# Optimization experiments

Hardware: AMD Instinct MI355X
Metric: run time of the kernel (lower is better)

Reference implementation:

```python
import jax, jax.numpy as jnp
import numpy as np

D, H, HD, F, L, V, R = 4096, 32, 128, 11008, 2, 32002, 64
ALPHA = 16.0
B, S = 2, 1024
EPS = 1e-5


def setup_inputs() -> dict:
    key = jax.random.key(0)
    ks = jax.random.split(key, 24)
    n = lambda k, shape: (jax.random.normal(k, shape, jnp.float32) * 0.02)
    return {
        "input_ids": jax.random.randint(ks[0], (B, S), 0, V),
        "attention_mask": jnp.ones((B, S), jnp.int32),
        "embed": n(ks[1], (V, D)),
        "Wq": n(ks[2], (L, D, D)), "Wk": n(ks[3], (L, D, D)),
        "Wv": n(ks[4], (L, D, D)), "Wo": n(ks[5], (L, D, D)),
        "Aq": n(ks[6], (L, R, D)), "Bq": jnp.zeros((L, D, R), jnp.float32),
        "Ak": n(ks[7], (L, R, D)), "Bk": n(ks[8], (L, D, R)),
        "Av": n(ks[9], (L, R, D)), "Bv": n(ks[10], (L, D, R)),
        "Ao": n(ks[11], (L, R, D)), "Bo": n(ks[12], (L, D, R)),
        "Wgate": n(ks[13], (L, F, D)), "Wup": n(ks[14], (L, F, D)),
        "Wdown": n(ks[15], (L, D, F)),
        "attn_norm_w": jnp.ones((L, D), jnp.float32),
        "mlp_norm_w": jnp.ones((L, D), jnp.float32),
        "final_norm_w": jnp.ones((D,), jnp.float32),
        "cls_W": n(ks[16], (3, D)), "cls_b": jnp.zeros((3,), jnp.float32),
    }


def _rmsnorm(x, w):
    var = jnp.mean(jnp.square(x), axis=-1, keepdims=True)
    return (x * jax.lax.rsqrt(var + EPS)) * w


def _rope(seq_len):
    inv = 1.0 / (10000.0 ** (jnp.arange(0, HD, 2, dtype=jnp.float32) / HD))
    freqs = jnp.outer(jnp.arange(seq_len, dtype=jnp.float32), inv)  # [S, HD/2]
    emb = jnp.concatenate([freqs, freqs], -1)  # [S, HD]
    return jnp.cos(emb), jnp.sin(emb)


def _rot_half(x):
    h = x.shape[-1] // 2
    return jnp.concatenate([-x[..., h:], x[..., :h]], -1)


def _lora(h, W, A, Bm):
    # h @ W.T + (alpha/r) * (h @ A.T) @ B.T   (dropout inactive in eval)
    return h @ W.T + (h @ A.T) @ Bm.T * (ALPHA / R)


def reference(input_ids, attention_mask, embed, Wq, Wk, Wv, Wo,
              Aq, Bq, Ak, Bk, Av, Bv, Ao, Bo,
              Wgate, Wup, Wdown, attn_norm_w, mlp_norm_w, final_norm_w,
              cls_W, cls_b):
    b, s = input_ids.shape
    x = embed[input_ids]  # [B,S,D]
    cos, sin = _rope(s)  # [S,HD]
    causal = jnp.tril(jnp.ones((s, s), bool))
    mask = causal[None, None] & (attention_mask[:, None, None, :] > 0)
    bias = jnp.where(mask, 0.0, -1e9).astype(jnp.float32)  # [B,1,S,S]

    def heads(t):  # [B,S,D] -> [B,H,S,HD]
        return t.reshape(b, s, H, HD).transpose(0, 2, 1, 3)

    for l in range(L):
        h = _rmsnorm(x, attn_norm_w[l])
        q = heads(_lora(h, Wq[l], Aq[l], Bq[l]))
        k = heads(_lora(h, Wk[l], Ak[l], Bk[l]))
        v = heads(_lora(h, Wv[l], Av[l], Bv[l]))
        q = q * cos + _rot_half(q) * sin
        k = k * cos + _rot_half(k) * sin
        scores = jnp.einsum('bhqd,bhkd->bhqk', q, k) / np.sqrt(HD) + bias
        attn = jax.nn.softmax(scores, axis=-1)
        o = jnp.einsum('bhqk,bhkd->bhqd', attn, v)
        o = o.transpose(0, 2, 1, 3).reshape(b, s, D)
        x = x + _lora(o, Wo[l], Ao[l], Bo[l])
        h = _rmsnorm(x, mlp_norm_w[l])
        x = x + (jax.nn.silu(h @ Wgate[l].T) * (h @ Wup[l].T)) @ Wdown[l].T

    x = _rmsnorm(x, final_norm_w)
    cls = x[:, 0, :]  # [CLS] at position 0 (right padding)
    return cls @ cls_W.T + cls_b
```

## Files before the change

### kernel.cpp

```cpp
#include <hip/hip_runtime.h>
#include <cstdint>
#include <cstddef>

#define D_   4096
#define H_   32
#define HD_  128
#define F_   11008
#define L_   2
#define R_   64
#define BB   2
#define SS   1024
#define TOK  (BB*SS)
#define N3   12288
#define EPS_ 1e-5f

typedef __attribute__((ext_vector_type(8))) short          s16x8;
typedef __attribute__((ext_vector_type(4))) float          fx4;
typedef __attribute__((ext_vector_type(4))) unsigned short u16x4t;
typedef __attribute__((ext_vector_type(8))) unsigned short u16x8t;

__device__ __forceinline__ unsigned short f2bf(float f) {
  union { float f; unsigned u; } x; x.f = f;
  unsigned r = (x.u + 0x7FFFu + ((x.u >> 16) & 1u)) >> 16;
  return (unsigned short)r;
}
__device__ __forceinline__ float b2f(unsigned short h) {
  union { unsigned u; float f; } x; x.u = ((unsigned)h) << 16;
  return x.f;
}

__device__ __forceinline__ void xcd_remap(int nwg, int mt_cnt, int& mt, int& nt) {
  const int orig = blockIdx.x;
  const int q = nwg >> 3, r = nwg & 7;
  const int xcd = orig & 7, i = orig >> 3;
  const int wgid = (xcd < r ? xcd * (q + 1) : r * (q + 1) + (xcd - r) * q) + i;
  mt = wgid % mt_cnt;
  nt = wgid / mt_cnt;
}

__global__ void k_embed(const int* __restrict__ ids, const float* __restrict__ emb,
                        float* __restrict__ x) {
  const int tok = blockIdx.x, tid = threadIdx.x;
  const int id = ids[tok];
  const float* s = emb + (size_t)id * D_;
  float* d = x + (size_t)tok * D_;
#pragma unroll
  for (int i = 0; i < 4; ++i)
    *(fx4*)(d + i * 1024 + tid * 4) = *(const fx4*)(s + i * 1024 + tid * 4);
}

__global__ __launch_bounds__(256) void k_cvt(const float* __restrict__ src,
                                             unsigned short* __restrict__ dst, int n) {
  const int stride = gridDim.x * 256 * 8;
  for (int i = (blockIdx.x * 256 + threadIdx.x) * 8; i < n; i += stride) {
    fx4 a = *(const fx4*)(src + i);
    fx4 b = *(const fx4*)(src + i + 4);
    u16x8t p;
    p[0] = f2bf(a[0]); p[1] = f2bf(a[1]); p[2] = f2bf(a[2]); p[3] = f2bf(a[3]);
    p[4] = f2bf(b[0]); p[5] = f2bf(b[1]); p[6] = f2bf(b[2]); p[7] = f2bf(b[3]);
    *(u16x8t*)(dst + i) = p;
  }
}

__global__ __launch_bounds__(256) void k_rmsnorm(const float* __restrict__ x,
                                                 const float* __restrict__ w,
                                                 unsigned short* __restrict__ out) {
  const int row = blockIdx.x, tid = threadIdx.x;
  const float* xr = x + (size_t)row * D_;
  fx4 v[4];
  float ss = 0.f;
#pragma unroll
  for (int i = 0; i < 4; ++i) {
    v[i] = *(const fx4*)(xr + i * 1024 + tid * 4);
    ss += v[i][0]*v[i][0] + v[i][1]*v[i][1] + v[i][2]*v[i][2] + v[i][3]*v[i][3];
  }
#pragma unroll
  for (int off = 32; off > 0; off >>= 1) ss += __shfl_down(ss, off);
  __shared__ float red[4];
  if ((tid & 63) == 0) red[tid >> 6] = ss;
  __syncthreads();
  const float sc = rsqrtf((red[0] + red[1] + red[2] + red[3]) * (1.f / D_) + EPS_);
  unsigned short* orow = out + (size_t)row * D_;
#pragma unroll
  for (int i = 0; i < 4; ++i) {
    fx4 wv = *(const fx4*)(w + i * 1024 + tid * 4);
    u16x4t pk;
    pk.x = f2bf(v[i][0] * sc * wv[0]);
    pk.y = f2bf(v[i][1] * sc * wv[1]);
    pk.z = f2bf(v[i][2] * sc * wv[2]);
    pk.w = f2bf(v[i][3] * sc * wv[3]);
    *(u16x4t*)(orow + i * 1024 + tid * 4) = pk;
  }
}

__global__ __launch_bounds__(256) void k_merge(const float* __restrict__ W,
                                               const float* __restrict__ Al,
                                               const float* __restrict__ Bl,
                                               unsigned short* __restrict__ Wm, int Kd) {
  __shared__ float sBm[64 * 64];
  __shared__ float sAl[64 * 68];
  const int tid = threadIdx.x;
  const int n0 = blockIdx.y * 64, k0 = blockIdx.x * 64;
#pragma unroll
  for (int it = 0; it < 4; ++it) {
    int e = it * 1024 + tid * 4;
    int row = e >> 6, col = e & 63;
    *(fx4*)&sBm[row * 64 + col] = *(const fx4*)(Bl + (size_t)(n0 + row) * 64 + col);
    *(fx4*)&sAl[row * 68 + col] = *(const fx4*)(Al + (size_t)row * Kd + k0 + col);
  }
  __syncthreads();
  const int lane = tid & 63, wave = tid >> 6;
  for (int nn = 0; nn < 16; ++nn) {
    int n = wave * 16 + nn;
    float a = 0.f;
#pragma unroll
    for (int r = 0; r < 64; ++r) a += sBm[n * 64 + r] * sAl[r * 68 + lane];
    size_t gi = (size_t)(n0 + n) * Kd + k0 + lane;
    Wm[gi] = f2bf(W[gi] + 0.25f * a);
  }
}

template <int EPI>
__global__ __launch_bounds__(256, 4) void k_gemm(const unsigned short* __restrict__ A,
                                                 const unsigned short* __restrict__ Wb,
                                                 float* __restrict__ outF,
                                                 unsigned short* __restrict__ outB,
                                                 const float* __restrict__ auxF,
                                                 int M, int N, int K, int nwg) {
  __shared__ unsigned short sA[128 * 64];
  __shared__ unsigned short sB[128 * 64];
  const int tid = threadIdx.x;
  const int wave = tid >> 6, lane = tid & 63;
  int mt, nt;
  xcd_remap(nwg, M >> 7, mt, nt);
  const int m0 = mt * 128, n0 = nt * 128;
  const int wr = wave >> 1, wc = wave & 1;
  const int l15 = lane & 15, l4 = lane >> 4;

  fx4 acc[4][4];
#pragma unroll
  for (int i = 0; i < 4; ++i)
#pragma unroll
    for (int j = 0; j < 4; ++j) acc[i][j] = (fx4){0.f, 0.f, 0.f, 0.f};

  const int nsteps = K >> 6;
  const int arow = tid >> 3;
  const int acol = (((tid & 7) ^ (arow & 7)) << 3);

  for (int t = 0; t < nsteps; ++t) {
    const int kb = t << 6;
#pragma unroll
    for (int i = 0; i < 4; ++i) {
      const unsigned short* gp = A + (size_t)(m0 + i * 32 + arow) * K + kb + acol;
      unsigned short* lp = sA + i * 2048 + wave * 512;
      __builtin_amdgcn_global_load_lds(
          (const __attribute__((address_space(1))) unsigned int*)gp,
          (__attribute__((address_space(3))) unsigned int*)lp, 16, 0, 0);
    }
#pragma unroll
    for (int i = 0; i < 4; ++i) {
      const unsigned short* gp = Wb + (size_t)(n0 + i * 32 + arow) * K + kb + acol;
      unsigned short* lp = sB + i * 2048 + wave * 512;
      __builtin_amdgcn_global_load_lds(
          (const __attribute__((address_space(1))) unsigned int*)gp,
          (__attribute__((address_space(3))) unsigned int*)lp, 16, 0, 0);
    }
    __syncthreads();
#pragma unroll
    for (int ks = 0; ks < 2; ++ks) {
      s16x8 af[4], bfr[4];
#pragma unroll
      for (int i = 0; i < 4; ++i) {
        int row = wr * 64 + i * 16 + l15;
        int cid = (((ks * 4) + l4) ^ (row & 7)) << 3;
        af[i] = *(const s16x8*)&sA[row * 64 + cid];
      }
#pragma unroll
      for (int j = 0; j < 4; ++j) {
        int row = wc * 64 + j * 16 + l15;
        int cid = (((ks * 4) + l4) ^ (row & 7)) << 3;
        bfr[j] = *(const s16x8*)&sB[row * 64 + cid];
      }
#pragma unroll
      for (int i = 0; i < 4; ++i)
#pragma unroll
        for (int j = 0; j < 4; ++j)
          acc[i][j] = __builtin_amdgcn_mfma_f32_16x16x32_bf16(af[i], bfr[j], acc[i][j], 0, 0, 0);
    }
    __syncthreads();
  }

  const int r0 = m0 + wr * 64 + (l4 << 2);
  const int c0 = n0 + wc * 64 + l15;
#pragma unroll
  for (int i = 0; i < 4; ++i)
#pragma unroll
    for (int j = 0; j < 4; ++j)
#pragma unroll
      for (int r = 0; r < 4; ++r) {
        size_t idx = (size_t)(r0 + i * 16 + r) * N + (c0 + j * 16);
        float v = acc[i][j][r];
        if (EPI == 2) outF[idx] = v + auxF[idx];
        else          outB[idx] = f2bf(v);
      }
}

__global__ __launch_bounds__(256, 2) void k_gemm_gu2(const unsigned short* __restrict__ A,
                                                     const unsigned short* __restrict__ Wg,
                                                     const unsigned short* __restrict__ Wu,
                                                     unsigned short* __restrict__ outB,
                                                     int M, int N, int K, int nwg) {
  __shared__ unsigned short sA[128 * 64];
  __shared__ unsigned short sG[128 * 64];
  __shared__ unsigned short sU[128 * 64];
  const int tid = threadIdx.x;
  const int wave = tid >> 6, lane = tid & 63;
  int mt, nt;
  xcd_remap(nwg, M >> 7, mt, nt);
  const int m0 = mt * 128, n0 = nt * 128;
  const int wr = wave >> 1, wc = wave & 1;
  const int l15 = lane & 15, l4 = lane >> 4;

  fx4 accg[4][4], accu[4][4];
#pragma unroll
  for (int i = 0; i < 4; ++i)
#pragma unroll
    for (int j = 0; j < 4; ++j) {
      accg[i][j] = (fx4){0.f, 0.f, 0.f, 0.f};
      accu[i][j] = (fx4){0.f, 0.f, 0.f, 0.f};
    }

  const int nsteps = K >> 6;
  const int arow = tid >> 3;
  const int acol = (((tid & 7) ^ (arow & 7)) << 3);

  for (int t = 0; t < nsteps; ++t) {
    const int kb = t << 6;
#pragma unroll
    for (int i = 0; i < 4; ++i) {
      const unsigned short* gp = A + (size_t)(m0 + i * 32 + arow) * K + kb + acol;
      unsigned short* lp = sA + i * 2048 + wave * 512;
      __builtin_amdgcn_global_load_lds(
          (const __attribute__((address_space(1))) unsigned int*)gp,
          (__attribute__((address_space(3))) unsigned int*)lp, 16, 0, 0);
    }
#pragma unroll
    for (int i = 0; i < 4; ++i) {
      const unsigned short* gp = Wg + (size_t)(n0 + i * 32 + arow) * K + kb + acol;
      unsigned short* lp = sG + i * 2048 + wave * 512;
      __builtin_amdgcn_global_load_lds(
          (const __attribute__((address_space(1))) unsigned int*)gp,
          (__attribute__((address_space(3))) unsigned int*)lp, 16, 0, 0);
    }
#pragma unroll
    for (int i = 0; i < 4; ++i) {
      const unsigned short* gp = Wu + (size_t)(n0 + i * 32 + arow) * K + kb + acol;
      unsigned short* lp = sU + i * 2048 + wave * 512;
      __builtin_amdgcn_global_load_lds(
          (const __attribute__((address_space(1))) unsigned int*)gp,
          (__attribute__((address_space(3))) unsigned int*)lp, 16, 0, 0);
    }
    __syncthreads();
#pragma unroll
    for (int ks = 0; ks < 2; ++ks) {
      s16x8 af[4], bg[4], bu[4];
#pragma unroll
      for (int i = 0; i < 4; ++i) {
        int row = wr * 64 + i * 16 + l15;
        int cid = (((ks * 4) + l4) ^ (row & 7)) << 3;
        af[i] = *(const s16x8*)&sA[row * 64 + cid];
      }
#pragma unroll
      for (int j = 0; j < 4; ++j) {
        int row = wc * 64 + j * 16 + l15;
        int cid = (((ks * 4) + l4) ^ (row & 7)) << 3;
        bg[j] = *(const s16x8*)&sG[row * 64 + cid];
        bu[j] = *(const s16x8*)&sU[row * 64 + cid];
      }
#pragma unroll
      for (int i = 0; i < 4; ++i)
#pragma unroll
        for (int j = 0; j < 4; ++j) {
          accg[i][j] = __builtin_amdgcn_mfma_f32_16x16x32_bf16(af[i], bg[j], accg[i][j], 0, 0, 0);
          accu[i][j] = __builtin_amdgcn_mfma_f32_16x16x32_bf16(af[i], bu[j], accu[i][j], 0, 0, 0);
        }
    }
    __syncthreads();
  }

  const int r0 = m0 + wr * 64 + (l4 << 2);
  const int c0 = n0 + wc * 64 + l15;
#pragma unroll
  for (int i = 0; i < 4; ++i)
#pragma unroll
    for (int j = 0; j < 4; ++j)
#pragma unroll
      for (int r = 0; r < 4; ++r) {
        size_t idx = (size_t)(r0 + i * 16 + r) * N + (c0 + j * 16);
        float g = accg[i][j][r];
        outB[idx] = f2bf(accu[i][j][r] * g / (1.f + __expf(-g)));
      }
}

__global__ void k_ropetab(float* __restrict__ cosT, float* __restrict__ sinT) {
  int idx = blockIdx.x * 256 + threadIdx.x;
  int s = idx >> 6, d = idx & 63;
  float inv = powf(10000.f, -(float)d * (1.f / 64.f));
  float f = (float)s * inv;
  cosT[idx] = cosf(f);
  sinT[idx] = sinf(f);
}

__global__ __launch_bounds__(256, 3) void k_attn(const unsigned short* __restrict__ P3,
                                                 const float* __restrict__ cosT,
                                                 const float* __restrict__ sinT,
                                                 const int* __restrict__ am,
                                                 unsigned short* __restrict__ O) {
  __shared__ unsigned short sK[64 * 136];
  __shared__ unsigned short sV[128 * 72];
  __shared__ unsigned short sP[4 * 16 * 72];
  const int tid = threadIdx.x, wave = tid >> 6, lane = tid & 63;
  const int bh = blockIdx.y, b = bh >> 5, h = bh & 31;
  const int qt = blockIdx.x;
  const float scale = 0.08838834764831845f;
  const int l15 = lane & 15, l4 = lane >> 4;

  const int qs = qt * 64 + wave * 16 + l15;
  s16x8 qf[4];
  {
    const unsigned short* qp = P3 + (size_t)(b * SS + qs) * N3 + h * HD_;
    const float* cr = cosT + qs * 64;
    const float* sr = sinT + qs * 64;
#pragma unroll
    for (int ks = 0; ks < 2; ++ks) {
      int dlo = ks * 32 + l4 * 8;
      u16x8t qlo = *(const u16x8t*)(qp + dlo);
      u16x8t qhi = *(const u16x8t*)(qp + dlo + 64);
      u16x8t plo, phi;
#pragma unroll
      for (int j = 0; j < 8; ++j) {
        float lo = b2f(qlo[j]), hi = b2f(qhi[j]);
        float c = cr[dlo + j], s = sr[dlo + j];
        plo[j] = f2bf(lo * c - hi * s);
        phi[j] = f2bf(hi * c + lo * s);
      }
      qf[ks]     = *(s16x8*)&plo;
      qf[ks + 2] = *(s16x8*)&phi;
    }
  }

  fx4 oacc[8];
#pragma unroll
  for (int nf = 0; nf < 8; ++nf) oacc[nf] = (fx4){0.f, 0.f, 0.f, 0.f};
  float mrun[4] = {-1e30f, -1e30f, -1e30f, -1e30f};
  float lrun[4] = {0.f, 0.f, 0.f, 0.f};

  const int ntiles = qt + 1;
  for (int kt = 0; kt < ntiles; ++kt) {
    const int k0 = kt * 64;
    __syncthreads();
    {
      int row = tid >> 2, part = tid & 3;
      int ksr = k0 + row;
      const unsigned short* kp = P3 + (size_t)(b * SS + ksr) * N3 + 4096 + h * HD_;
      const float* cr = cosT + ksr * 64;
      const float* sr = sinT + ksr * 64;
#pragma unroll
      for (int g = 0; g < 2; ++g) {
        int d0 = part * 16 + g * 8;
        u16x8t klo = *(const u16x8t*)(kp + d0);
        u16x8t khi = *(const u16x8t*)(kp + d0 + 64);
        u16x8t wlo, whi;
#pragma unroll
        for (int j = 0; j < 8; ++j) {
          float lo = b2f(klo[j]), hi = b2f(khi[j]);
          float c = cr[d0 + j], s = sr[d0 + j];
          wlo[j] = f2bf(lo * c - hi * s);
          whi[j] = f2bf(hi * c + lo * s);
        }
        *(u16x8t*)&sK[row * 136 + d0]      = wlo;
        *(u16x8t*)&sK[row * 136 + d0 + 64] = whi;
      }
    }
    {
#pragma unroll
      for (int it = 0; it < 8; ++it) {
        int key = it * 8 + (tid >> 5), hd0 = (tid & 31) * 4;
        u16x4t v = *(const u16x4t*)(P3 + (size_t)(b * SS + k0 + key) * N3 + 8192 + h * HD_ + hd0);
        sV[(hd0 + 0) * 72 + key] = v.x;
        sV[(hd0 + 1) * 72 + key] = v.y;
        sV[(hd0 + 2) * 72 + key] = v.z;
        sV[(hd0 + 3) * 72 + key] = v.w;
      }
    }
    __syncthreads();
    if (k0 <= qt * 64 + wave * 16 + 15) {
      fx4 sfr[4];
#pragma unroll
      for (int kf = 0; kf < 4; ++kf) sfr[kf] = (fx4){0.f, 0.f, 0.f, 0.f};
#pragma unroll
      for (int kf = 0; kf < 4; ++kf)
#pragma unroll
        for (int ks = 0; ks < 4; ++ks) {
          s16x8 kfr = *(const s16x8*)&sK[(kf * 16 + l15) * 136 + ks * 32 + l4 * 8];
          sfr[kf] = __builtin_amdgcn_mfma_f32_16x16x32_bf16(qf[ks], kfr, sfr[kf], 0, 0, 0);
        }
      float p[16], corr[4];
#pragma unroll
      for (int r = 0; r < 4; ++r) {
        int qr = qt * 64 + wave * 16 + l4 * 4 + r;
        float mx = -1e30f;
#pragma unroll
        for (int kf = 0; kf < 4; ++kf) {
          int key = k0 + kf * 16 + l15;
          float bb = (key <= qr && am[b * SS + key] != 0) ? 0.f : -1e9f;
          p[kf * 4 + r] = sfr[kf][r] * scale + bb;
          mx = fmaxf(mx, p[kf * 4 + r]);
        }
        mx = fmaxf(mx, __shfl_xor(mx, 1));
        mx = fmaxf(mx, __shfl_xor(mx, 2));
        mx = fmaxf(mx, __shfl_xor(mx, 4));
        mx = fmaxf(mx, __shfl_xor(mx, 8));
        float mn = fmaxf(mrun[r], mx);
        corr[r] = __expf(mrun[r] - mn);
        mrun[r] = mn;
        float rs = 0.f;
#pragma unroll
        for (int kf = 0; kf < 4; ++kf) {
          p[kf * 4 + r] = __expf(p[kf * 4 + r] - mn);
          rs += p[kf * 4 + r];
        }
        rs += __shfl_xor(rs, 1);
        rs += __shfl_xor(rs, 2);
        rs += __shfl_xor(rs, 4);
        rs += __shfl_xor(rs, 8);
        lrun[r] = lrun[r] * corr[r] + rs;
      }
#pragma unroll
      for (int nf = 0; nf < 8; ++nf) {
        oacc[nf][0] *= corr[0];
        oacc[nf][1] *= corr[1];
        oacc[nf][2] *= corr[2];
        oacc[nf][3] *= corr[3];
      }
      unsigned short* pp = sP + wave * (16 * 72);
#pragma unroll
      for (int r = 0; r < 4; ++r) {
        int row = l4 * 4 + r;
#pragma unroll
        for (int kf = 0; kf < 4; ++kf)
          pp[row * 72 + kf * 16 + l15] = f2bf(p[kf * 4 + r]);
      }
      s16x8 pa0 = *(const s16x8*)&pp[l15 * 72 + l4 * 8];
      s16x8 pa1 = *(const s16x8*)&pp[l15 * 72 + 32 + l4 * 8];
#pragma unroll
      for (int nf = 0; nf < 8; ++nf) {
        s16x8 v0 = *(const s16x8*)&sV[(nf * 16 + l15) * 72 + l4 * 8];
        s16x8 v1 = *(const s16x8*)&sV[(nf * 16 + l15) * 72 + 32 + l4 * 8];
        oacc[nf] = __builtin_amdgcn_mfma_f32_16x16x32_bf16(pa0, v0, oacc[nf], 0, 0, 0);
        oacc[nf] = __builtin_amdgcn_mfma_f32_16x16x32_bf16(pa1, v1, oacc[nf], 0, 0, 0);
      }
    }
  }
  const size_t obase = (size_t)b * SS * D_ + h * HD_;
#pragma unroll
  for (int nf = 0; nf < 8; ++nf)
#pragma unroll
    for (int r = 0; r < 4; ++r) {
      int qr = qt * 64 + wave * 16 + l4 * 4 + r;
      O[obase + (size_t)qr * D_ + nf * 16 + l15] = f2bf(oacc[nf][r] / lrun[r]);
    }
}

__global__ __launch_bounds__(256) void k_final(const float* __restrict__ xf,
                                               const float* __restrict__ fw,
                                               const float* __restrict__ cW,
                                               const float* __restrict__ cb,
                                               float* __restrict__ out) {
  const int b = blockIdx.x, tid = threadIdx.x;
  const float* xr = xf + (size_t)b * SS * D_;
  __shared__ float red[4];
  fx4 v[4];
  float ss = 0.f;
#pragma unroll
  for (int i = 0; i < 4; ++i) {
    v[i] = *(const fx4*)(xr + i * 1024 + tid * 4);
    ss += v[i][0]*v[i][0] + v[i][1]*v[i][1] + v[i][2]*v[i][2] + v[i][3]*v[i][3];
  }
#pragma unroll
  for (int off = 32; off > 0; off >>= 1) ss += __shfl_down(ss, off);
  if ((tid & 63) == 0) red[tid >> 6] = ss;
  __syncthreads();
  const float sc = rsqrtf((red[0] + red[1] + red[2] + red[3]) * (1.f / D_) + EPS_);
  for (int c = 0; c < 3; ++c) {
    float d = 0.f;
#pragma unroll
    for (int i = 0; i < 4; ++i) {
      fx4 fv = *(const fx4*)(fw + i * 1024 + tid * 4);
      fx4 cw = *(const fx4*)(cW + (size_t)c * D_ + i * 1024 + tid * 4);
#pragma unroll
      for (int j = 0; j < 4; ++j) d += v[i][j] * sc * fv[j] * cw[j];
    }
#pragma unroll
    for (int off = 32; off > 0; off >>= 1) d += __shfl_down(d, off);
    __syncthreads();
    if ((tid & 63) == 0) red[tid >> 6] = d;
    __syncthreads();
    if (tid == 0) out[b * 3 + c] = red[0] + red[1] + red[2] + red[3] + cb[c];
  }
}

extern "C" void kernel_launch(void* const* d_in, const int* in_sizes, int n_in,
                              void* d_out, int out_size, void* d_ws, size_t ws_size,
                              hipStream_t stream) {
  const int*   ids = (const int*)d_in[0];
  const int*   am  = (const int*)d_in[1];
  const float* emb = (const float*)d_in[2];
  const float* Wq  = (const float*)d_in[3];
  const float* Wk  = (const float*)d_in[4];
  const float* Wv  = (const float*)d_in[5];
  const float* Wo  = (const float*)d_in[6];
  const float* Aq  = (const float*)d_in[7];
  const float* Bq  = (const float*)d_in[8];
  const float* Ak  = (const float*)d_in[9];
  const float* Bk  = (const float*)d_in[10];
  const float* Av  = (const float*)d_in[11];
  const float* Bv  = (const float*)d_in[12];
  const float* Ao  = (const float*)d_in[13];
  const float* Bo  = (const float*)d_in[14];
  const float* Wg  = (const float*)d_in[15];
  const float* Wu  = (const float*)d_in[16];
  const float* Wd  = (const float*)d_in[17];
  const float* anw = (const float*)d_in[18];
  const float* mnw = (const float*)d_in[19];
  const float* fnw = (const float*)d_in[20];
  const float* cW  = (const float*)d_in[21];
  const float* cb  = (const float*)d_in[22];
  float* out = (float*)d_out;

  char* w = (char*)d_ws;
  float* xf = (float*)w;                     w += (size_t)TOK * D_ * 4;
  unsigned short* P3 = (unsigned short*)w;   w += (size_t)TOK * N3 * 2;
  unsigned short* gact = (unsigned short*)w; w += (size_t)TOK * F_ * 2;
  unsigned short* hb = (unsigned short*)w;   w += (size_t)TOK * D_ * 2;
  unsigned short* ob = (unsigned short*)w;   w += (size_t)TOK * D_ * 2;
  unsigned short* Wm3 = (unsigned short*)w;  w += (size_t)3 * D_ * D_ * 2;
  unsigned short* Wgu = (unsigned short*)w;  w += (size_t)2 * F_ * D_ * 2;
  float* cosT = (float*)w;                   w += (size_t)SS * 64 * 4;
  float* sinT = (float*)w;                   w += (size_t)SS * 64 * 4;
  if ((size_t)(w - (char*)d_ws) > ws_size) return;

  k_ropetab<<<256, 256, 0, stream>>>(cosT, sinT);
  k_embed<<<TOK, 256, 0, stream>>>(ids, emb, xf);

  const int nwgQKV = (N3 / 128) * (TOK / 128);
  const int nwgProj = (D_ / 128) * (TOK / 128);
  const int nwgMlp = (F_ / 128) * (TOK / 128);
  dim3 gMerge(D_ / 64, D_ / 64);
  dim3 gAttn(SS / 64, BB * H_);
  const int CVT_BLK = 2048;

  for (int l = 0; l < L_; ++l) {
    const size_t oDD = (size_t)l * D_ * D_;
    const size_t oRD = (size_t)l * R_ * D_;
    const size_t oDR = (size_t)l * D_ * R_;
    const size_t oFD = (size_t)l * F_ * D_;

    k_rmsnorm<<<TOK, 256, 0, stream>>>(xf, anw + (size_t)l * D_, hb);
    k_merge<<<gMerge, 256, 0, stream>>>(Wq + oDD, Aq + oRD, Bq + oDR, Wm3, D_);
    k_merge<<<gMerge, 256, 0, stream>>>(Wk + oDD, Ak + oRD, Bk + oDR, Wm3 + (size_t)D_ * D_, D_);
    k_merge<<<gMerge, 256, 0, stream>>>(Wv + oDD, Av + oRD, Bv + oDR, Wm3 + (size_t)2 * D_ * D_, D_);
    k_gemm<5><<<nwgQKV, 256, 0, stream>>>(hb, Wm3, nullptr, P3, nullptr, TOK, N3, D_, nwgQKV);
    k_attn<<<gAttn, 256, 0, stream>>>(P3, cosT, sinT, am, ob);
    k_merge<<<gMerge, 256, 0, stream>>>(Wo + oDD, Ao + oRD, Bo + oDR, Wm3, D_);
    k_gemm<2><<<nwgProj, 256, 0, stream>>>(ob, Wm3, xf, nullptr, xf, TOK, D_, D_, nwgProj);
    k_rmsnorm<<<TOK, 256, 0, stream>>>(xf, mnw + (size_t)l * D_, hb);
    k_cvt<<<CVT_BLK, 256, 0, stream>>>(Wg + oFD, Wgu, F_ * D_);
    k_cvt<<<CVT_BLK, 256, 0, stream>>>(Wu + oFD, Wgu + (size_t)F_ * D_, F_ * D_);
    k_gemm_gu2<<<nwgMlp, 256, 0, stream>>>(hb, Wgu, Wgu + (size_t)F_ * D_, gact, TOK, F_, D_, nwgMlp);
    k_cvt<<<CVT_BLK, 256, 0, stream>>>(Wd + oFD, Wgu, D_ * F_);
    k_gemm<2><<<nwgProj, 256, 0, stream>>>(gact, Wgu, xf, nullptr, xf, TOK, D_, F_, nwgProj);
  }

  k_final<<<BB, 256, 0, stream>>>(xf, fnw, cW, cb, out);
  (void)in_sizes; (void)n_in; (void)out_size;
}
```

Before: 3.250 ms.

## Replace LoRA weight merging with low-rank activation path fused into GEMM tail

Instead of merging B·A into each dense weight (a rank-64 outer product over D×D per projection), the code converts W to bf16 directly and computes h·Aᵀ with a split-K kernel and a reduction. It then appends the rank-64 term as one extra K-step inside the main GEMM using bf16 B matrices. The attention grid is also reversed so heavier causal tiles launch first, and GEMM occupancy hint is raised. This adds several small kernels and partial-sum buffers, and the rank term gets an extra bf16 rounding step.

```diff
diff --git a/kernel.cpp b/kernel.cpp
--- a/kernel.cpp
+++ b/kernel.cpp
@@ -93,39 +93,86 @@
   }
 }
 
-__global__ __launch_bounds__(256) void k_merge(const float* __restrict__ W,
-                                               const float* __restrict__ Al,
-                                               const float* __restrict__ Bl,
-                                               unsigned short* __restrict__ Wm, int Kd) {
-  __shared__ float sBm[64 * 64];
-  __shared__ float sAl[64 * 68];
-  const int tid = threadIdx.x;
-  const int n0 = blockIdx.y * 64, k0 = blockIdx.x * 64;
-#pragma unroll
-  for (int it = 0; it < 4; ++it) {
-    int e = it * 1024 + tid * 4;
-    int row = e >> 6, col = e & 63;
-    *(fx4*)&sBm[row * 64 + col] = *(const fx4*)(Bl + (size_t)(n0 + row) * 64 + col);
-    *(fx4*)&sAl[row * 68 + col] = *(const fx4*)(Al + (size_t)row * Kd + k0 + col);
-  }
-  __syncthreads();
-  const int lane = tid & 63, wave = tid >> 6;
-  for (int nn = 0; nn < 16; ++nn) {
-    int n = wave * 16 + nn;
-    float a = 0.f;
-#pragma unroll
-    for (int r = 0; r < 64; ++r) a += sBm[n * 64 + r] * sAl[r * 68 + lane];
-    size_t gi = (size_t)(n0 + n) * Kd + k0 + lane;
-    Wm[gi] = f2bf(W[gi] + 0.25f * a);
-  }
-}
-
-template <int EPI>
-__global__ __launch_bounds__(256, 4) void k_gemm(const unsigned short* __restrict__ A,
+template <int NFRAG>
+__global__ __launch_bounds__(256, 2) void k_lmid(const unsigned short* __restrict__ Ain,
+                                                 const float* __restrict__ P0,
+                                                 const float* __restrict__ P1,
+                                                 const float* __restrict__ P2,
+                                                 float* __restrict__ part) {
+  __shared__ unsigned short sA[64 * 64];
+  __shared__ unsigned short sW[NFRAG * 16 * 72];
+  const int tid = threadIdx.x, wave = tid >> 6, lane = tid & 63;
+  const int l15 = lane & 15, l4 = lane >> 4;
+  const int m0 = blockIdx.x * 64;
+  const int kbase = blockIdx.y * 512;
+  const int arow = tid >> 3;
+  const int acol = (((tid & 7) ^ (arow & 7)) << 3);
+  const int brow = tid >> 4;
+  const int bcol = (tid & 15) << 2;
+  const float* ptrs[3] = {P0, P1, P2};
+
+  fx4 acc[NFRAG];
+#pragma unroll
+  for (int j = 0; j < NFRAG; ++j) acc[j] = (fx4){0.f, 0.f, 0.f, 0.f};
+
+  for (int t = 0; t < 8; ++t) {
+    const int kb = kbase + t * 64;
+#pragma unroll
+    for (int i = 0; i < 2; ++i) {
+      const unsigned short* gp = Ain + (size_t)(m0 + i * 32 + arow) * 4096 + kb + acol;
+      unsigned short* lp = sA + i * 2048 + wave * 512;
+      __builtin_amdgcn_global_load_lds(
+          (const __attribute__((address_space(1))) unsigned int*)gp,
+          (__attribute__((address_space(3))) unsigned int*)lp, 16, 0, 0);
+    }
+#pragma unroll
+    for (int j = 0; j < NFRAG; ++j) {
+      const float* wp = ptrs[j >> 2] + (size_t)((j & 3) * 16 + brow) * 4096 + kb + bcol;
+      fx4 v = *(const fx4*)wp;
+      u16x4t pk;
+      pk.x = f2bf(v[0]); pk.y = f2bf(v[1]); pk.z = f2bf(v[2]); pk.w = f2bf(v[3]);
+      *(u16x4t*)&sW[(j * 16 + brow) * 72 + bcol] = pk;
+    }
+    __syncthreads();
+#pragma unroll
+    for (int ks = 0; ks < 2; ++ks) {
+      const int row = wave * 16 + l15;
+      const int cid = (((ks * 4) + l4) ^ (row & 7)) << 3;
+      s16x8 af = *(const s16x8*)&sA[row * 64 + cid];
+#pragma unroll
+      for (int j = 0; j < NFRAG; ++j) {
+        s16x8 bf = *(const s16x8*)&sW[(j * 16 + l15) * 72 + ks * 32 + (l4 << 3)];
+        acc[j] = __builtin_amdgcn_mfma_f32_16x16x32_bf16(af, bf, acc[j], 0, 0, 0);
+      }
+    }
+    __syncthreads();
+  }
+  const size_t base = (size_t)blockIdx.y * 2048 * (NFRAG * 16);
+#pragma unroll
+  for (int j = 0; j < NFRAG; ++j)
+#pragma unroll
+    for (int r = 0; r < 4; ++r)
+      part[base + (size_t)(m0 + wave * 16 + l4 * 4 + r) * (NFRAG * 16) + j * 16 + l15] = acc[j][r];
+}
+
+__global__ void k_lmred(const float* __restrict__ part, unsigned short* __restrict__ outb, int ld) {
+  const int idx = blockIdx.x * 256 + threadIdx.x;
+  const int stride = 2048 * ld;
+  float s = 0.f;
+#pragma unroll
+  for (int ks = 0; ks < 8; ++ks) s += part[(size_t)ks * stride + idx];
+  outb[idx] = f2bf(0.25f * s);
+}
+
+template <int EPI, bool EXT>
+__global__ __launch_bounds__(256, 5) void k_gemm(const unsigned short* __restrict__ A,
                                                  const unsigned short* __restrict__ Wb,
                                                  float* __restrict__ outF,
                                                  unsigned short* __restrict__ outB,
                                                  const float* __restrict__ auxF,
+                                                 const unsigned short* __restrict__ Aext,
+                                                 int ldaE,
+                                                 const unsigned short* __restrict__ Wext,
                                                  int M, int N, int K, int nwg) {
   __shared__ unsigned short sA[128 * 64];
   __shared__ unsigned short sB[128 * 64];
@@ -188,6 +235,50 @@
           acc[i][j] = __builtin_amdgcn_mfma_f32_16x16x32_bf16(af[i], bfr[j], acc[i][j], 0, 0, 0);
     }
     __syncthreads();
+  }
+
+  if constexpr (EXT) {
+    const int third = n0 >> 12;
+    const unsigned short* Ae = Aext + third * 64;
+    const unsigned short* We = Wext + (size_t)n0 * 64;
+#pragma unroll
+    for (int i = 0; i < 4; ++i) {
+      const unsigned short* gp = Ae + (size_t)(m0 + i * 32 + arow) * ldaE + acol;
+      unsigned short* lp = sA + i * 2048 + wave * 512;
+      __builtin_amdgcn_global_load_lds(
+          (const __attribute__((address_space(1))) unsigned int*)gp,
+          (__attribute__((address_space(3))) unsigned int*)lp, 16, 0, 0);
+    }
+#pragma unroll
+    for (int i = 0; i < 4; ++i) {
+      const unsigned short* gp = We + (size_t)(i * 32 + arow) * 64 + acol;
+      unsigned short* lp = sB + i * 2048 + wave * 512;
+      __builtin_amdgcn_global_load_lds(
+          (const __attribute__((address_space(1))) unsigned int*)gp,
+          (__attribute__((address_space(3))) unsigned int*)lp, 16, 0, 0);
+    }
+    __syncthreads();
+#pragma unroll
+    for (int ks = 0; ks < 2; ++ks) {
+      s16x8 af[4], bfr[4];
+#pragma unroll
+      for (int i = 0; i < 4; ++i) {
+        int row = wr * 64 + i * 16 + l15;
+        int cid = (((ks * 4) + l4) ^ (row & 7)) << 3;
+        af[i] = *(const s16x8*)&sA[row * 64 + cid];
+      }
+#pragma unroll
+      for (int j = 0; j < 4; ++j) {
+        int row = wc * 64 + j * 16 + l15;
+        int cid = (((ks * 4) + l4) ^ (row & 7)) << 3;
+        bfr[j] = *(const s16x8*)&sB[row * 64 + cid];
+      }
+#pragma unroll
+      for (int i = 0; i < 4; ++i)
+#pragma unroll
+        for (int j = 0; j < 4; ++j)
+          acc[i][j] = __builtin_amdgcn_mfma_f32_16x16x32_bf16(af[i], bfr[j], acc[i][j], 0, 0, 0);
+    }
   }
 
   const int r0 = m0 + wr * 64 + (l4 << 2);
@@ -321,7 +412,7 @@
   __shared__ unsigned short sP[4 * 16 * 72];
   const int tid = threadIdx.x, wave = tid >> 6, lane = tid & 63;
   const int bh = blockIdx.y, b = bh >> 5, h = bh & 31;
-  const int qt = blockIdx.x;
+  const int qt = (int)gridDim.x - 1 - blockIdx.x;
   const float scale = 0.08838834764831845f;
   const int l15 = lane & 15, l4 = lane >> 4;
 
@@ -546,6 +637,12 @@
   unsigned short* ob = (unsigned short*)w;   w += (size_t)TOK * D_ * 2;
   unsigned short* Wm3 = (unsigned short*)w;  w += (size_t)3 * D_ * D_ * 2;
   unsigned short* Wgu = (unsigned short*)w;  w += (size_t)2 * F_ * D_ * 2;
+  unsigned short* Bx3 = (unsigned short*)w;  w += (size_t)3 * D_ * R_ * 2;
+  unsigned short* BxO = (unsigned short*)w;  w += (size_t)D_ * R_ * 2;
+  unsigned short* lm3 = (unsigned short*)w;  w += (size_t)TOK * 192 * 2;
+  unsigned short* lmo = (unsigned short*)w;  w += (size_t)TOK * 64 * 2;
+  float* lm3p = (float*)w;                   w += (size_t)8 * TOK * 192 * 4;
+  float* lmop = (float*)w;                   w += (size_t)8 * TOK * 64 * 4;
   float* cosT = (float*)w;                   w += (size_t)SS * 64 * 4;
   float* sinT = (float*)w;                   w += (size_t)SS * 64 * 4;
   if ((size_t)(w - (char*)d_ws) > ws_size) return;
@@ -556,8 +653,8 @@
   const int nwgQKV = (N3 / 128) * (TOK / 128);
   const int nwgProj = (D_ / 128) * (TOK / 128);
   const int nwgMlp = (F_ / 128) * (TOK / 128);
-  dim3 gMerge(D_ / 64, D_ / 64);
   dim3 gAttn(SS / 64, BB * H_);
+  dim3 gLmid(TOK / 64, 8);
   const int CVT_BLK = 2048;
 
   for (int l = 0; l < L_; ++l) {
@@ -567,19 +664,30 @@
     const size_t oFD = (size_t)l * F_ * D_;
 
     k_rmsnorm<<<TOK, 256, 0, stream>>>(xf, anw + (size_t)l * D_, hb);
-    k_merge<<<gMerge, 256, 0, stream>>>(Wq + oDD, Aq + oRD, Bq + oDR, Wm3, D_);
-    k_merge<<<gMerge, 256, 0, stream>>>(Wk + oDD, Ak + oRD, Bk + oDR, Wm3 + (size_t)D_ * D_, D_);
-    k_merge<<<gMerge, 256, 0, stream>>>(Wv + oDD, Av + oRD, Bv + oDR, Wm3 + (size_t)2 * D_ * D_, D_);
-    k_gemm<5><<<nwgQKV, 256, 0, stream>>>(hb, Wm3, nullptr, P3, nullptr, TOK, N3, D_, nwgQKV);
+    k_cvt<<<CVT_BLK, 256, 0, stream>>>(Wq + oDD, Wm3, D_ * D_);
+    k_cvt<<<CVT_BLK, 256, 0, stream>>>(Wk + oDD, Wm3 + (size_t)D_ * D_, D_ * D_);
+    k_cvt<<<CVT_BLK, 256, 0, stream>>>(Wv + oDD, Wm3 + (size_t)2 * D_ * D_, D_ * D_);
+    k_cvt<<<128, 256, 0, stream>>>(Bq + oDR, Bx3, D_ * R_);
+    k_cvt<<<128, 256, 0, stream>>>(Bk + oDR, Bx3 + (size_t)D_ * R_, D_ * R_);
+    k_cvt<<<128, 256, 0, stream>>>(Bv + oDR, Bx3 + (size_t)2 * D_ * R_, D_ * R_);
+    k_lmid<12><<<gLmid, 256, 0, stream>>>(hb, Aq + oRD, Ak + oRD, Av + oRD, lm3p);
+    k_lmred<<<TOK * 192 / 256, 256, 0, stream>>>(lm3p, lm3, 192);
+    k_gemm<5, true><<<nwgQKV, 256, 0, stream>>>(hb, Wm3, nullptr, P3, nullptr,
+                                                lm3, 192, Bx3, TOK, N3, D_, nwgQKV);
     k_attn<<<gAttn, 256, 0, stream>>>(P3, cosT, sinT, am, ob);
-    k_merge<<<gMerge, 256, 0, stream>>>(Wo + oDD, Ao + oRD, Bo + oDR, Wm3, D_);
-    k_gemm<2><<<nwgProj, 256, 0, stream>>>(ob, Wm3, xf, nullptr, xf, TOK, D_, D_, nwgProj);
+    k_cvt<<<CVT_BLK, 256, 0, stream>>>(Wo + oDD, Wm3, D_ * D_);
+    k_cvt<<<128, 256, 0, stream>>>(Bo + oDR, BxO, D_ * R_);
+    k_lmid<4><<<gLmid, 256, 0, stream>>>(ob, Ao + oRD, Ao + oRD, Ao + oRD, lmop);
+    k_lmred<<<TOK * 64 / 256, 256, 0, stream>>>(lmop, lmo, 64);
+    k_gemm<2, true><<<nwgProj, 256, 0, stream>>>(ob, Wm3, xf, nullptr, xf,
+                                                 lmo, 64, BxO, TOK, D_, D_, nwgProj);
     k_rmsnorm<<<TOK, 256, 0, stream>>>(xf, mnw + (size_t)l * D_, hb);
     k_cvt<<<CVT_BLK, 256, 0, stream>>>(Wg + oFD, Wgu, F_ * D_);
     k_cvt<<<CVT_BLK, 256, 0, stream>>>(Wu + oFD, Wgu + (size_t)F_ * D_, F_ * D_);
     k_gemm_gu2<<<nwgMlp, 256, 0, stream>>>(hb, Wgu, Wgu + (size_t)F_ * D_, gact, TOK, F_, D_, nwgMlp);
     k_cvt<<<CVT_BLK, 256, 0, stream>>>(Wd + oFD, Wgu, D_ * F_);
-    k_gemm<2><<<nwgProj, 256, 0, stream>>>(gact, Wgu, xf, nullptr, xf, TOK, D_, F_, nwgProj);
+    k_gemm<2, false><<<nwgProj, 256, 0, stream>>>(gact, Wgu, xf, nullptr, xf,
+                                                  nullptr, 0, nullptr, TOK, D_, F_, nwgProj);
   }
 
   k_final<<<BB, 256, 0, stream>>>(xf, fnw, cW, cb, out);
```

Result: slower. 4.497 ms (+38.4%).
